# Kernel optimization log

Hardware: AMD Instinct MI355X
Metric: run time of the kernel (lower is better)

## Reference

```python
import jax, jax.numpy as jnp
import numpy as np

D_MODEL = 1024
N_HEAD = 16
D_K = D_MODEL // N_HEAD
B, S = 2, 2048
NEG = -1000000000.0


def setup_inputs() -> dict:
    key = jax.random.key(0)
    ks = jax.random.split(key, 9)
    inp = {
        "input_q": jax.random.normal(ks[0], (B, S, D_MODEL), dtype=jnp.float32),
        "input_k": jax.random.normal(ks[1], (B, S, D_MODEL), dtype=jnp.float32),
        "input_v": jax.random.normal(ks[2], (B, S, D_MODEL), dtype=jnp.float32),
        "mask": jax.random.randint(ks[3], (1, 1, S, S), 0, 2, dtype=jnp.int32),
        # parameters (Linear weights stored as [in, out] for x @ W)
        "w_q": jax.random.normal(ks[4], (D_MODEL, D_MODEL), dtype=jnp.float32) / np.sqrt(D_MODEL),
        "w_k": jax.random.normal(ks[5], (D_MODEL, D_MODEL), dtype=jnp.float32) / np.sqrt(D_MODEL),
        "w_v": jax.random.normal(ks[6], (D_MODEL, D_MODEL), dtype=jnp.float32) / np.sqrt(D_MODEL),
        "w_o": jax.random.normal(ks[7], (D_MODEL, D_MODEL), dtype=jnp.float32) / np.sqrt(D_MODEL),
        "b_o": jax.random.normal(ks[8], (D_MODEL,), dtype=jnp.float32) * 0.01,
    }
    return inp


def reference(input_q, input_k, input_v, mask, w_q, w_k, w_v, w_o, b_o):
    b = input_q.shape[0]
    # QKV projections -> [B, H, S, d_k]
    def split_heads(x):
        return x.reshape(b, -1, N_HEAD, D_K).transpose(0, 2, 1, 3)
    q = split_heads(input_q @ w_q)
    k = split_heads(input_k @ w_k)
    v = split_heads(input_v @ w_v)
    # naive attention: materialize [B, H, Sq, Sk] scores
    scores = jnp.einsum("bhqd,bhkd->bhqk", q, k) / jnp.sqrt(jnp.float32(D_K))
    scores = jnp.where(mask == 0, jnp.float32(NEG), scores)
    attn = jax.nn.softmax(scores, axis=-1)
    per_head = jnp.einsum("bhqk,bhkd->bhqd", attn, v)
    concat = per_head.transpose(0, 2, 1, 3).reshape(b, -1, N_HEAD * D_K)
    return concat @ w_o + b_o
```

## Files before the change

### kernel.cpp

```cpp
#include <hip/hip_runtime.h>
#include <hip/hip_bf16.h>

typedef _Float16 halfx8 __attribute__((ext_vector_type(8)));
typedef _Float16 halfx4 __attribute__((ext_vector_type(4)));
typedef _Float16 half2t __attribute__((ext_vector_type(2)));
typedef __fp16 fp16x2 __attribute__((ext_vector_type(2)));
typedef float floatx4 __attribute__((ext_vector_type(4)));

constexpr int S = 2048;
constexpr int DM = 1024;
constexpr int NH = 16;
constexpr int DK = 64;
constexpr int BATCH = 2;
constexpr int MROWS = 4096;
constexpr float QSCALE = 0.125f * 1.44269504088896340736f;

#if defined(__has_builtin)
#if __has_builtin(__builtin_amdgcn_fdot2)
#define HAVE_FDOT2 1
#endif
#if __has_builtin(__builtin_amdgcn_exp2f)
#define EXP2F(x) __builtin_amdgcn_exp2f(x)
#endif
#endif
#ifndef EXP2F
#define EXP2F(x) __builtin_exp2f(x)
#endif

static __device__ inline half2t pack2(float a, float b) {
  return __builtin_bit_cast(half2t, __builtin_amdgcn_cvt_pkrtz(a, b));
}

static __device__ inline float hdot2(half2t a, half2t b, float c) {
#ifdef HAVE_FDOT2
  return __builtin_amdgcn_fdot2(__builtin_bit_cast(fp16x2, a),
                                __builtin_bit_cast(fp16x2, b), c, false);
#else
  return c + (float)a[0] * (float)b[0] + (float)a[1] * (float)b[1];
#endif
}

static __device__ inline void load_lds16(const _Float16* g, _Float16* l) {
  __builtin_amdgcn_global_load_lds((const __attribute__((address_space(1))) void*)g,
                                   (__attribute__((address_space(3))) void*)l, 16, 0, 0);
}

__global__ void convert_w4(const float* __restrict__ w0, const float* __restrict__ w1,
                           const float* __restrict__ w2, const float* __restrict__ w3,
                           _Float16* __restrict__ o0, _Float16* __restrict__ o1,
                           _Float16* __restrict__ o2, _Float16* __restrict__ o3) {
  const float* w = (blockIdx.z == 0) ? w0 : (blockIdx.z == 1) ? w1 : (blockIdx.z == 2) ? w2 : w3;
  _Float16* wt = (blockIdx.z == 0) ? o0 : (blockIdx.z == 1) ? o1 : (blockIdx.z == 2) ? o2 : o3;
  __shared__ float tile[32][33];
  int n0 = blockIdx.x * 32, k0 = blockIdx.y * 32;
  int tx = threadIdx.x, ty = threadIdx.y;
#pragma unroll
  for (int i = 0; i < 4; ++i)
    tile[ty + i * 8][tx] = w[(k0 + ty + i * 8) * DM + n0 + tx];
  __syncthreads();
#pragma unroll
  for (int i = 0; i < 4; ++i)
    wt[(n0 + ty + i * 8) * DM + k0 + tx] = (_Float16)tile[tx][ty + i * 8];
}

__global__ void convert_in3(const float* __restrict__ a0, const float* __restrict__ a1,
                            const float* __restrict__ a2, _Float16* __restrict__ o0,
                            _Float16* __restrict__ o1, _Float16* __restrict__ o2) {
  const float* a = (blockIdx.z == 0) ? a0 : (blockIdx.z == 1) ? a1 : a2;
  _Float16* o = (blockIdx.z == 0) ? o0 : (blockIdx.z == 1) ? o1 : o2;
  size_t i = ((size_t)blockIdx.x * 256 + threadIdx.x) * 8;
  float4 va = *(const float4*)(a + i);
  float4 vb = *(const float4*)(a + i + 4);
  union { halfx8 v; _Float16 h[8]; } u;
  u.h[0] = (_Float16)va.x; u.h[1] = (_Float16)va.y;
  u.h[2] = (_Float16)va.z; u.h[3] = (_Float16)va.w;
  u.h[4] = (_Float16)vb.x; u.h[5] = (_Float16)vb.y;
  u.h[6] = (_Float16)vb.z; u.h[7] = (_Float16)vb.w;
  *(halfx8*)(o + i) = u.v;
}

__global__ void mask_swz(const int* __restrict__ m, _Float16* __restrict__ Mt) {
  int t = blockIdx.x * 256 + threadIdx.x;
  int j0 = (t & 1) * 8;
  int quad = (t >> 1) & 3;
  int q = (t >> 3) & (S - 1);
  int kt = t >> 14;
  const int* src = m + (size_t)q * S + kt * 64 + (j0 >> 2) * 16 + quad * 4;
  int4 a = *(const int4*)src;
  int4 b = *(const int4*)(src + 16);
  union { halfx8 v; _Float16 h[8]; } u;
  u.h[0] = (_Float16)(a.x != 0); u.h[1] = (_Float16)(a.y != 0);
  u.h[2] = (_Float16)(a.z != 0); u.h[3] = (_Float16)(a.w != 0);
  u.h[4] = (_Float16)(b.x != 0); u.h[5] = (_Float16)(b.y != 0);
  u.h[6] = (_Float16)(b.z != 0); u.h[7] = (_Float16)(b.w != 0);
  *(halfx8*)(Mt + (size_t)t * 8) = u.v;
}

__global__ __launch_bounds__(256) void qkv_gemm(const _Float16* __restrict__ xq,
                                                const _Float16* __restrict__ xk,
                                                const _Float16* __restrict__ xv,
                                                const _Float16* __restrict__ wqkv,
                                                _Float16* __restrict__ Qf,
                                                _Float16* __restrict__ Kf,
                                                _Float16* __restrict__ Vt) {
  __shared__ __align__(16) _Float16 smem[17408];
  _Float16* Asm = smem;
  _Float16* Bsm = smem + 128 * 64;
  const int tid = threadIdx.x;
  const int w = tid >> 6, l = tid & 63, lo = l & 15, quad = l >> 4;
  const int lo7 = l & 7;
  const int wm = (w >> 1) * 64, wn = (w & 1) * 64;
  const int bx = blockIdx.x, bm = blockIdx.y * 128;
  const int wid = bx >> 3;
  const _Float16* A = (wid == 0) ? xq : (wid == 1) ? xk : xv;
  const _Float16* Bt = wqkv + (size_t)bx * 128 * DM;

  floatx4 acc[4][4] = {};

  for (int k0 = 0; k0 < DM; k0 += 64) {
#pragma unroll
    for (int i = 0; i < 4; ++i) {
      int chunk = i * 256 + tid;
      int r = chunk >> 3;
      int c = (chunk & 7) ^ (r & 7);
      load_lds16(A + (size_t)(bm + r) * DM + k0 + c * 8, Asm + chunk * 8);
    }
#pragma unroll
    for (int i = 0; i < 4; ++i) {
      int chunk = i * 256 + tid;
      int r = chunk >> 3;
      int c = (chunk & 7) ^ (r & 7);
      load_lds16(Bt + (size_t)r * DM + k0 + c * 8, Bsm + chunk * 8);
    }
    __syncthreads();

#pragma unroll
    for (int ks = 0; ks < 2; ++ks) {
      halfx8 af[4], bf[4];
#pragma unroll
      for (int mt = 0; mt < 4; ++mt)
        af[mt] = *(const halfx8*)&Asm[(wm + mt * 16 + lo) * 64 + (((ks * 4 + quad) ^ lo7) * 8)];
#pragma unroll
      for (int nt = 0; nt < 4; ++nt)
        bf[nt] = *(const halfx8*)&Bsm[(wn + nt * 16 + lo) * 64 + (((ks * 4 + quad) ^ lo7) * 8)];
#pragma unroll
      for (int mt = 0; mt < 4; ++mt)
#pragma unroll
        for (int nt = 0; nt < 4; ++nt)
          acc[mt][nt] =
              __builtin_amdgcn_mfma_f32_16x16x32_f16(af[mt], bf[nt], acc[mt][nt], 0, 0, 0);
    }
    __syncthreads();
  }

  if (wid == 2) {
    constexpr int LDTT = 136;
    _Float16* tb = smem;
#pragma unroll
    for (int mt = 0; mt < 4; ++mt)
#pragma unroll
      for (int nt = 0; nt < 4; ++nt)
#pragma unroll
        for (int r = 0; r < 4; ++r) {
          int dl = wn + nt * 16 + lo;
          int sl = wm + mt * 16 + quad * 4 + r;
          tb[dl * LDTT + sl] = (_Float16)acc[mt][nt][r];
        }
    __syncthreads();
    const int b = bm >> 11, s0 = bm & (S - 1);
    const int d2 = tid >> 1, chunk = (tid & 1) * 64;
    const int dg = ((bx & 7) * 128 + d2);
    const int h = dg >> 6, dd = dg & 63;
    _Float16* O = Vt + ((size_t)(b * NH + h) * DK + dd) * S + s0 + chunk;
#pragma unroll
    for (int j = 0; j < 8; ++j)
      *(halfx8*)(O + j * 8) = *(const halfx8*)&tb[d2 * LDTT + chunk + j * 8];
    return;
  }

  _Float16* Out = (wid == 0) ? Qf : Kf;
  const float scale = (wid == 0) ? QSCALE : 1.0f;
#pragma unroll
  for (int mt = 0; mt < 4; ++mt)
#pragma unroll
    for (int nt = 0; nt < 4; ++nt)
#pragma unroll
      for (int r = 0; r < 4; ++r) {
        int row = bm + wm + mt * 16 + quad * 4 + r;
        int col = (bx & 7) * 128 + wn + nt * 16 + lo;
        Out[(size_t)row * DM + col] = (_Float16)(acc[mt][nt][r] * scale);
      }
}

__global__ __launch_bounds__(256, 2) void attn_kernel(const _Float16* __restrict__ Qf,
                                                      const _Float16* __restrict__ Kf,
                                                      const _Float16* __restrict__ Vt,
                                                      const _Float16* __restrict__ Mt,
                                                      _Float16* __restrict__ concat) {
  __shared__ __align__(16) _Float16 K0s[64 * 64], K1s[64 * 64];
  __shared__ __align__(16) _Float16 V0s[64 * 64], V1s[64 * 64];
  __shared__ __align__(16) _Float16 Psm[4 * 32 * 64];

  const int tid = threadIdx.x;
  const int w = tid >> 6, l = tid & 63, lo = l & 15, quad = l >> 4, lo7 = l & 7;
  const int qb = blockIdx.x * 128 + w * 32;
  const int h = blockIdx.y, b = blockIdx.z;

  const _Float16* Kbase = Kf + (size_t)b * S * DM + h * DK;
  const _Float16* Vb = Vt + (size_t)(b * NH + h) * DK * S;
  _Float16* Pw = Psm + w * 32 * 64;

  const int r0 = tid >> 3, c0 = (tid & 7) ^ (r0 & 7);
  const int r1 = (256 + tid) >> 3, c1 = ((256 + tid) & 7) ^ (r1 & 7);

  halfx8 qf[2][2];
  const _Float16* Mp[2];
#pragma unroll
  for (int g = 0; g < 2; ++g) {
#pragma unroll
    for (int ks = 0; ks < 2; ++ks)
      qf[g][ks] = *(const halfx8*)(Qf + ((size_t)b * S + qb + g * 16 + lo) * DM + h * DK +
                                   ks * 32 + quad * 8);
    Mp[g] = Mt + ((size_t)(qb + g * 16 + lo) * 4 + quad) * 16;
  }

  floatx4 Oacc[2][4] = {};
  float lsum[2] = {0.f, 0.f};
  const half2t onev = {(_Float16)1.0f, (_Float16)1.0f};

  auto stage = [&](int kt, _Float16* Kd, _Float16* Vd) {
    load_lds16(Kbase + (size_t)(kt * 64 + r0) * DM + c0 * 8, Kd + tid * 8);
    load_lds16(Vb + (size_t)r0 * S + kt * 64 + c0 * 8, Vd + tid * 8);
    load_lds16(Kbase + (size_t)(kt * 64 + r1) * DM + c1 * 8, Kd + (256 + tid) * 8);
    load_lds16(Vb + (size_t)r1 * S + kt * 64 + c1 * 8, Vd + (256 + tid) * 8);
  };

  auto tile = [&](const _Float16* Kc, const _Float16* Vc, const halfx8* mc) {
    floatx4 Sacc[2][4] = {};
#pragma unroll
    for (int ks = 0; ks < 2; ++ks)
#pragma unroll
      for (int nt = 0; nt < 4; ++nt) {
        halfx8 kf = *(const halfx8*)&Kc[(nt * 16 + lo) * 64 + (((ks * 4 + quad) ^ lo7) * 8)];
        Sacc[0][nt] = __builtin_amdgcn_mfma_f32_16x16x32_f16(kf, qf[0][ks], Sacc[0][nt], 0, 0, 0);
        Sacc[1][nt] = __builtin_amdgcn_mfma_f32_16x16x32_f16(kf, qf[1][ks], Sacc[1][nt], 0, 0, 0);
      }
#pragma unroll
    for (int g = 0; g < 2; ++g) {
      union { halfx8 v; half2t h2[4]; } mu0, mu1;
      mu0.v = mc[g * 2];
      mu1.v = mc[g * 2 + 1];
      half2t mm[8] = {mu0.h2[0], mu0.h2[1], mu0.h2[2], mu0.h2[3],
                      mu1.h2[0], mu1.h2[1], mu1.h2[2], mu1.h2[3]};
#pragma unroll
      for (int nt = 0; nt < 4; ++nt) {
        half2t p01 = pack2(EXP2F(Sacc[g][nt][0]), EXP2F(Sacc[g][nt][1]));
        half2t p23 = pack2(EXP2F(Sacc[g][nt][2]), EXP2F(Sacc[g][nt][3]));
        p01 *= mm[nt * 2];
        p23 *= mm[nt * 2 + 1];
        lsum[g] = hdot2(p01, onev, lsum[g]);
        lsum[g] = hdot2(p23, onev, lsum[g]);
        union { halfx4 v; half2t hh[2]; } u;
        u.hh[0] = p01;
        u.hh[1] = p23;
        *(halfx4*)&Pw[(g * 16 + lo) * 64 + (((2 * nt + (quad >> 1)) ^ lo7) * 8) +
                      (quad & 1) * 4] = u.v;
      }
    }
#pragma unroll
    for (int ks = 0; ks < 2; ++ks) {
      halfx8 pf0 = *(const halfx8*)&Pw[lo * 64 + (((ks * 4 + quad) ^ lo7) * 8)];
      halfx8 pf1 = *(const halfx8*)&Pw[(16 + lo) * 64 + (((ks * 4 + quad) ^ lo7) * 8)];
#pragma unroll
      for (int nt = 0; nt < 4; ++nt) {
        halfx8 vf = *(const halfx8*)&Vc[(nt * 16 + lo) * 64 + (((ks * 4 + quad) ^ lo7) * 8)];
        Oacc[0][nt] = __builtin_amdgcn_mfma_f32_16x16x32_f16(pf0, vf, Oacc[0][nt], 0, 0, 0);
        Oacc[1][nt] = __builtin_amdgcn_mfma_f32_16x16x32_f16(pf1, vf, Oacc[1][nt], 0, 0, 0);
      }
    }
  };

  halfx8 mr[4];
#pragma unroll
  for (int g = 0; g < 2; ++g) {
    mr[g * 2] = *(const halfx8*)(Mp[g]);
    mr[g * 2 + 1] = *(const halfx8*)(Mp[g] + 8);
  }
  stage(0, K0s, V0s);

  for (int kt = 0; kt < S / 64; kt += 2) {
    __syncthreads();
    stage(kt + 1, K1s, V1s);
    halfx8 mc[4] = {mr[0], mr[1], mr[2], mr[3]};
#pragma unroll
    for (int g = 0; g < 2; ++g) {
      mr[g * 2] = *(const halfx8*)(Mp[g] + (size_t)(kt + 1) * 131072);
      mr[g * 2 + 1] = *(const halfx8*)(Mp[g] + (size_t)(kt + 1) * 131072 + 8);
    }
    tile(K0s, V0s, mc);
    __syncthreads();
    if (kt + 2 < S / 64) stage(kt + 2, K0s, V0s);
    mc[0] = mr[0]; mc[1] = mr[1]; mc[2] = mr[2]; mc[3] = mr[3];
    if (kt + 2 < S / 64) {
#pragma unroll
      for (int g = 0; g < 2; ++g) {
        mr[g * 2] = *(const halfx8*)(Mp[g] + (size_t)(kt + 2) * 131072);
        mr[g * 2 + 1] = *(const halfx8*)(Mp[g] + (size_t)(kt + 2) * 131072 + 8);
      }
    }
    tile(K1s, V1s, mc);
  }

#pragma unroll
  for (int g = 0; g < 2; ++g) {
    lsum[g] += __shfl_xor(lsum[g], 16);
    lsum[g] += __shfl_xor(lsum[g], 32);
  }

#pragma unroll
  for (int g = 0; g < 2; ++g)
#pragma unroll
    for (int r = 0; r < 4; ++r) {
      float lr = __shfl(lsum[g], quad * 4 + r);
      float inv = __builtin_amdgcn_rcpf(lr);
      int q = qb + g * 16 + quad * 4 + r;
#pragma unroll
      for (int nt = 0; nt < 4; ++nt) {
        int d = nt * 16 + lo;
        concat[((size_t)b * S + q) * DM + h * DK + d] = (_Float16)(Oacc[g][nt][r] * inv);
      }
    }
}

__global__ __launch_bounds__(256) void out_gemm(const _Float16* __restrict__ A,
                                                const _Float16* __restrict__ Bt,
                                                float* __restrict__ Cp,
                                                const float* __restrict__ bias) {
  __shared__ __align__(16) _Float16 A0s[128 * 64], A1s[128 * 64];
  __shared__ __align__(16) _Float16 B0s[128 * 64], B1s[128 * 64];
  const int tid = threadIdx.x;
  const int w = tid >> 6, l = tid & 63, lo = l & 15, quad = l >> 4, lo7 = l & 7;
  const int wm = (w >> 1) * 64, wn = (w & 1) * 64;
  const int bm = blockIdx.y * 128, bn = blockIdx.x * 128;

  floatx4 acc[4][4] = {};

  auto stageg = [&](int k0, _Float16* Ad, _Float16* Bd) {
#pragma unroll
    for (int i = 0; i < 4; ++i) {
      int chunk = i * 256 + tid;
      int rr = chunk >> 3;
      int cc = (chunk & 7) ^ (rr & 7);
      load_lds16(A + (size_t)(bm + rr) * DM + k0 + cc * 8, Ad + chunk * 8);
      load_lds16(Bt + (size_t)(bn + rr) * DM + k0 + cc * 8, Bd + chunk * 8);
    }
  };
  auto comp = [&](const _Float16* As, const _Float16* Bs) {
#pragma unroll
    for (int ks = 0; ks < 2; ++ks) {
      halfx8 af[4], bf[4];
#pragma unroll
      for (int mt = 0; mt < 4; ++mt)
        af[mt] = *(const halfx8*)&As[(wm + mt * 16 + lo) * 64 + (((ks * 4 + quad) ^ lo7) * 8)];
#pragma unroll
      for (int nt = 0; nt < 4; ++nt)
        bf[nt] = *(const halfx8*)&Bs[(wn + nt * 16 + lo) * 64 + (((ks * 4 + quad) ^ lo7) * 8)];
#pragma unroll
      for (int mt = 0; mt < 4; ++mt)
#pragma unroll
        for (int nt = 0; nt < 4; ++nt)
          acc[mt][nt] =
              __builtin_amdgcn_mfma_f32_16x16x32_f16(af[mt], bf[nt], acc[mt][nt], 0, 0, 0);
    }
  };

  stageg(0, A0s, B0s);
  for (int k0 = 0; k0 < DM; k0 += 128) {
    __syncthreads();
    stageg(k0 + 64, A1s, B1s);
    comp(A0s, B0s);
    __syncthreads();
    if (k0 + 128 < DM) stageg(k0 + 128, A0s, B0s);
    comp(A1s, B1s);
  }

  float bv[4];
#pragma unroll
  for (int nt = 0; nt < 4; ++nt) bv[nt] = bias[bn + wn + nt * 16 + lo];
#pragma unroll
  for (int mt = 0; mt < 4; ++mt)
#pragma unroll
    for (int nt = 0; nt < 4; ++nt)
#pragma unroll
      for (int r = 0; r < 4; ++r) {
        int row = bm + wm + mt * 16 + quad * 4 + r;
        int col = bn + wn + nt * 16 + lo;
        Cp[(size_t)row * DM + col] = acc[mt][nt][r] + bv[nt];
      }
}

extern "C" void kernel_launch(void* const* d_in, const int* in_sizes, int n_in,
                              void* d_out, int out_size, void* d_ws, size_t ws_size,
                              hipStream_t stream) {
  const float* in_q = (const float*)d_in[0];
  const float* in_k = (const float*)d_in[1];
  const float* in_v = (const float*)d_in[2];
  const int* mask = (const int*)d_in[3];
  const float* w_q = (const float*)d_in[4];
  const float* w_k = (const float*)d_in[5];
  const float* w_v = (const float*)d_in[6];
  const float* w_o = (const float*)d_in[7];
  const float* b_o = (const float*)d_in[8];
  float* out = (float*)d_out;

  char* ws = (char*)d_ws;
  constexpr size_t WB = (size_t)DM * DM * sizeof(_Float16);
  constexpr size_t MB_ = (size_t)S * S * sizeof(_Float16);
  constexpr size_t TB = (size_t)MROWS * DM * sizeof(_Float16);
  _Float16* wqkv = (_Float16*)(ws);
  _Float16* wto = (_Float16*)(ws + 3 * WB);
  _Float16* Mt = (_Float16*)(ws + 4 * WB);
  char* p = ws + 4 * WB + MB_;
  _Float16* Qf = (_Float16*)(p);
  _Float16* Kf = (_Float16*)(p + TB);
  _Float16* Vt = (_Float16*)(p + 2 * TB);
  _Float16* xq = (_Float16*)(p + 3 * TB);
  _Float16* xk = (_Float16*)(p + 4 * TB);
  _Float16* xv = (_Float16*)(p + 5 * TB);
  _Float16* concat = xq;

  convert_w4<<<dim3(32, 32, 4), dim3(32, 8), 0, stream>>>(
      w_q, w_k, w_v, w_o, wqkv, wqkv + DM * DM, wqkv + 2 * DM * DM, wto);
  convert_in3<<<dim3(MROWS * DM / 8 / 256, 1, 3), 256, 0, stream>>>(in_q, in_k, in_v,
                                                                    xq, xk, xv);
  mask_swz<<<dim3(S * S / 8 / 256), 256, 0, stream>>>(mask, Mt);

  qkv_gemm<<<dim3(24, 32), 256, 0, stream>>>(xq, xk, xv, wqkv, Qf, Kf, Vt);
  attn_kernel<<<dim3(S / 128, NH, BATCH), 256, 0, stream>>>(Qf, Kf, Vt, Mt, concat);
  out_gemm<<<dim3(DM / 128, MROWS / 128), 256, 0, stream>>>(concat, wto, out, b_o);
}
```

Measured before the change: 250.7 us.

## Merge prep kernels and shrink attention and output-GEMM tiles for more blocks

Merges the three preprocessing kernels (weight transpose/convert, input convert, mask swizzle) into one launch that dispatches on block index, which removes two kernel launches. Cuts the attention block from 4 to 2 waves (64 query rows per block), doubling the grid to 1024 blocks, and narrows the output GEMM tile from 128 to 64 columns, doubling its grid to 512 blocks. The goal is better CU fill on a 256-CU part. The cost is less K/V and A-tile reuse per block and more global traffic.

```diff
diff --git a/kernel.cpp b/kernel.cpp
--- a/kernel.cpp
+++ b/kernel.cpp
@@ -45,55 +45,65 @@
                                    (__attribute__((address_space(3))) void*)l, 16, 0, 0);
 }
 
-__global__ void convert_w4(const float* __restrict__ w0, const float* __restrict__ w1,
-                           const float* __restrict__ w2, const float* __restrict__ w3,
-                           _Float16* __restrict__ o0, _Float16* __restrict__ o1,
-                           _Float16* __restrict__ o2, _Float16* __restrict__ o3) {
-  const float* w = (blockIdx.z == 0) ? w0 : (blockIdx.z == 1) ? w1 : (blockIdx.z == 2) ? w2 : w3;
-  _Float16* wt = (blockIdx.z == 0) ? o0 : (blockIdx.z == 1) ? o1 : (blockIdx.z == 2) ? o2 : o3;
+__global__ __launch_bounds__(256) void prep(const float* __restrict__ w_q,
+                                            const float* __restrict__ w_k,
+                                            const float* __restrict__ w_v,
+                                            const float* __restrict__ w_o,
+                                            _Float16* __restrict__ wqkv,
+                                            _Float16* __restrict__ wto,
+                                            const float* __restrict__ in_q,
+                                            const float* __restrict__ in_k,
+                                            const float* __restrict__ in_v,
+                                            _Float16* __restrict__ xq,
+                                            _Float16* __restrict__ xk,
+                                            _Float16* __restrict__ xv,
+                                            const int* __restrict__ mask,
+                                            _Float16* __restrict__ Mt) {
   __shared__ float tile[32][33];
-  int n0 = blockIdx.x * 32, k0 = blockIdx.y * 32;
-  int tx = threadIdx.x, ty = threadIdx.y;
-#pragma unroll
-  for (int i = 0; i < 4; ++i)
-    tile[ty + i * 8][tx] = w[(k0 + ty + i * 8) * DM + n0 + tx];
-  __syncthreads();
-#pragma unroll
-  for (int i = 0; i < 4; ++i)
-    wt[(n0 + ty + i * 8) * DM + k0 + tx] = (_Float16)tile[tx][ty + i * 8];
-}
-
-__global__ void convert_in3(const float* __restrict__ a0, const float* __restrict__ a1,
-                            const float* __restrict__ a2, _Float16* __restrict__ o0,
-                            _Float16* __restrict__ o1, _Float16* __restrict__ o2) {
-  const float* a = (blockIdx.z == 0) ? a0 : (blockIdx.z == 1) ? a1 : a2;
-  _Float16* o = (blockIdx.z == 0) ? o0 : (blockIdx.z == 1) ? o1 : o2;
-  size_t i = ((size_t)blockIdx.x * 256 + threadIdx.x) * 8;
-  float4 va = *(const float4*)(a + i);
-  float4 vb = *(const float4*)(a + i + 4);
-  union { halfx8 v; _Float16 h[8]; } u;
-  u.h[0] = (_Float16)va.x; u.h[1] = (_Float16)va.y;
-  u.h[2] = (_Float16)va.z; u.h[3] = (_Float16)va.w;
-  u.h[4] = (_Float16)vb.x; u.h[5] = (_Float16)vb.y;
-  u.h[6] = (_Float16)vb.z; u.h[7] = (_Float16)vb.w;
-  *(halfx8*)(o + i) = u.v;
-}
-
-__global__ void mask_swz(const int* __restrict__ m, _Float16* __restrict__ Mt) {
-  int t = blockIdx.x * 256 + threadIdx.x;
-  int j0 = (t & 1) * 8;
-  int quad = (t >> 1) & 3;
-  int q = (t >> 3) & (S - 1);
-  int kt = t >> 14;
-  const int* src = m + (size_t)q * S + kt * 64 + (j0 >> 2) * 16 + quad * 4;
-  int4 a = *(const int4*)src;
-  int4 b = *(const int4*)(src + 16);
-  union { halfx8 v; _Float16 h[8]; } u;
-  u.h[0] = (_Float16)(a.x != 0); u.h[1] = (_Float16)(a.y != 0);
-  u.h[2] = (_Float16)(a.z != 0); u.h[3] = (_Float16)(a.w != 0);
-  u.h[4] = (_Float16)(b.x != 0); u.h[5] = (_Float16)(b.y != 0);
-  u.h[6] = (_Float16)(b.z != 0); u.h[7] = (_Float16)(b.w != 0);
-  *(halfx8*)(Mt + (size_t)t * 8) = u.v;
+  const int bid = blockIdx.x;
+  const int tid = threadIdx.x;
+  if (bid < 4096) {
+    int wsel = bid >> 10, t = bid & 1023;
+    const float* w = (wsel == 0) ? w_q : (wsel == 1) ? w_k : (wsel == 2) ? w_v : w_o;
+    _Float16* wt = (wsel < 3) ? (wqkv + (size_t)wsel * DM * DM) : wto;
+    int n0 = (t & 31) * 32, k0 = (t >> 5) * 32;
+    int tx = tid & 31, ty = tid >> 5;
+#pragma unroll
+    for (int i = 0; i < 4; ++i)
+      tile[ty + i * 8][tx] = w[(size_t)(k0 + ty + i * 8) * DM + n0 + tx];
+    __syncthreads();
+#pragma unroll
+    for (int i = 0; i < 4; ++i)
+      wt[(size_t)(n0 + ty + i * 8) * DM + k0 + tx] = (_Float16)tile[tx][ty + i * 8];
+  } else if (bid < 10240) {
+    int idx = bid - 4096, isel = idx >> 11, blk = idx & 2047;
+    const float* a = (isel == 0) ? in_q : (isel == 1) ? in_k : in_v;
+    _Float16* o = (isel == 0) ? xq : (isel == 1) ? xk : xv;
+    size_t i = ((size_t)blk * 256 + tid) * 8;
+    float4 va = *(const float4*)(a + i);
+    float4 vb = *(const float4*)(a + i + 4);
+    union { halfx8 v; _Float16 h[8]; } u;
+    u.h[0] = (_Float16)va.x; u.h[1] = (_Float16)va.y;
+    u.h[2] = (_Float16)va.z; u.h[3] = (_Float16)va.w;
+    u.h[4] = (_Float16)vb.x; u.h[5] = (_Float16)vb.y;
+    u.h[6] = (_Float16)vb.z; u.h[7] = (_Float16)vb.w;
+    *(halfx8*)(o + i) = u.v;
+  } else {
+    int t = (bid - 10240) * 256 + tid;
+    int j0 = (t & 1) * 8;
+    int quad = (t >> 1) & 3;
+    int q = (t >> 3) & (S - 1);
+    int kt = t >> 14;
+    const int* src = mask + (size_t)q * S + kt * 64 + (j0 >> 2) * 16 + quad * 4;
+    int4 a = *(const int4*)src;
+    int4 b = *(const int4*)(src + 16);
+    union { halfx8 v; _Float16 h[8]; } u;
+    u.h[0] = (_Float16)(a.x != 0); u.h[1] = (_Float16)(a.y != 0);
+    u.h[2] = (_Float16)(a.z != 0); u.h[3] = (_Float16)(a.w != 0);
+    u.h[4] = (_Float16)(b.x != 0); u.h[5] = (_Float16)(b.y != 0);
+    u.h[6] = (_Float16)(b.z != 0); u.h[7] = (_Float16)(b.w != 0);
+    *(halfx8*)(Mt + (size_t)t * 8) = u.v;
+  }
 }
 
 __global__ __launch_bounds__(256) void qkv_gemm(const _Float16* __restrict__ xq,
@@ -192,26 +202,23 @@
       }
 }
 
-__global__ __launch_bounds__(256, 2) void attn_kernel(const _Float16* __restrict__ Qf,
+__global__ __launch_bounds__(128, 2) void attn_kernel(const _Float16* __restrict__ Qf,
                                                       const _Float16* __restrict__ Kf,
                                                       const _Float16* __restrict__ Vt,
                                                       const _Float16* __restrict__ Mt,
                                                       _Float16* __restrict__ concat) {
   __shared__ __align__(16) _Float16 K0s[64 * 64], K1s[64 * 64];
   __shared__ __align__(16) _Float16 V0s[64 * 64], V1s[64 * 64];
-  __shared__ __align__(16) _Float16 Psm[4 * 32 * 64];
+  __shared__ __align__(16) _Float16 Psm[2 * 32 * 64];
 
   const int tid = threadIdx.x;
   const int w = tid >> 6, l = tid & 63, lo = l & 15, quad = l >> 4, lo7 = l & 7;
-  const int qb = blockIdx.x * 128 + w * 32;
+  const int qb = blockIdx.x * 64 + w * 32;
   const int h = blockIdx.y, b = blockIdx.z;
 
   const _Float16* Kbase = Kf + (size_t)b * S * DM + h * DK;
   const _Float16* Vb = Vt + (size_t)(b * NH + h) * DK * S;
   _Float16* Pw = Psm + w * 32 * 64;
-
-  const int r0 = tid >> 3, c0 = (tid & 7) ^ (r0 & 7);
-  const int r1 = (256 + tid) >> 3, c1 = ((256 + tid) & 7) ^ (r1 & 7);
 
   halfx8 qf[2][2];
   const _Float16* Mp[2];
@@ -229,10 +236,14 @@
   const half2t onev = {(_Float16)1.0f, (_Float16)1.0f};
 
   auto stage = [&](int kt, _Float16* Kd, _Float16* Vd) {
-    load_lds16(Kbase + (size_t)(kt * 64 + r0) * DM + c0 * 8, Kd + tid * 8);
-    load_lds16(Vb + (size_t)r0 * S + kt * 64 + c0 * 8, Vd + tid * 8);
-    load_lds16(Kbase + (size_t)(kt * 64 + r1) * DM + c1 * 8, Kd + (256 + tid) * 8);
-    load_lds16(Vb + (size_t)r1 * S + kt * 64 + c1 * 8, Vd + (256 + tid) * 8);
+#pragma unroll
+    for (int i = 0; i < 4; ++i) {
+      int chunk = i * 128 + tid;
+      int r = chunk >> 3;
+      int c = (chunk & 7) ^ (r & 7);
+      load_lds16(Kbase + (size_t)(kt * 64 + r) * DM + c * 8, Kd + chunk * 8);
+      load_lds16(Vb + (size_t)r * S + kt * 64 + c * 8, Vd + chunk * 8);
+    }
   };
 
   auto tile = [&](const _Float16* Kc, const _Float16* Vc, const halfx8* mc) {
@@ -337,13 +348,13 @@
                                                 float* __restrict__ Cp,
                                                 const float* __restrict__ bias) {
   __shared__ __align__(16) _Float16 A0s[128 * 64], A1s[128 * 64];
-  __shared__ __align__(16) _Float16 B0s[128 * 64], B1s[128 * 64];
+  __shared__ __align__(16) _Float16 B0s[64 * 64], B1s[64 * 64];
   const int tid = threadIdx.x;
   const int w = tid >> 6, l = tid & 63, lo = l & 15, quad = l >> 4, lo7 = l & 7;
-  const int wm = (w >> 1) * 64, wn = (w & 1) * 64;
-  const int bm = blockIdx.y * 128, bn = blockIdx.x * 128;
-
-  floatx4 acc[4][4] = {};
+  const int wm = (w >> 1) * 64, wn = (w & 1) * 32;
+  const int bm = blockIdx.y * 128, bn = blockIdx.x * 64;
+
+  floatx4 acc[4][2] = {};
 
   auto stageg = [&](int k0, _Float16* Ad, _Float16* Bd) {
 #pragma unroll
@@ -352,23 +363,29 @@
       int rr = chunk >> 3;
       int cc = (chunk & 7) ^ (rr & 7);
       load_lds16(A + (size_t)(bm + rr) * DM + k0 + cc * 8, Ad + chunk * 8);
+    }
+#pragma unroll
+    for (int i = 0; i < 2; ++i) {
+      int chunk = i * 256 + tid;
+      int rr = chunk >> 3;
+      int cc = (chunk & 7) ^ (rr & 7);
       load_lds16(Bt + (size_t)(bn + rr) * DM + k0 + cc * 8, Bd + chunk * 8);
     }
   };
   auto comp = [&](const _Float16* As, const _Float16* Bs) {
 #pragma unroll
     for (int ks = 0; ks < 2; ++ks) {
-      halfx8 af[4], bf[4];
+      halfx8 af[4], bf[2];
 #pragma unroll
       for (int mt = 0; mt < 4; ++mt)
         af[mt] = *(const halfx8*)&As[(wm + mt * 16 + lo) * 64 + (((ks * 4 + quad) ^ lo7) * 8)];
 #pragma unroll
-      for (int nt = 0; nt < 4; ++nt)
+      for (int nt = 0; nt < 2; ++nt)
         bf[nt] = *(const halfx8*)&Bs[(wn + nt * 16 + lo) * 64 + (((ks * 4 + quad) ^ lo7) * 8)];
 #pragma unroll
       for (int mt = 0; mt < 4; ++mt)
 #pragma unroll
-        for (int nt = 0; nt < 4; ++nt)
+        for (int nt = 0; nt < 2; ++nt)
           acc[mt][nt] =
               __builtin_amdgcn_mfma_f32_16x16x32_f16(af[mt], bf[nt], acc[mt][nt], 0, 0, 0);
     }
@@ -384,13 +401,13 @@
     comp(A1s, B1s);
   }
 
-  float bv[4];
-#pragma unroll
-  for (int nt = 0; nt < 4; ++nt) bv[nt] = bias[bn + wn + nt * 16 + lo];
+  float bv[2];
+#pragma unroll
+  for (int nt = 0; nt < 2; ++nt) bv[nt] = bias[bn + wn + nt * 16 + lo];
 #pragma unroll
   for (int mt = 0; mt < 4; ++mt)
 #pragma unroll
-    for (int nt = 0; nt < 4; ++nt)
+    for (int nt = 0; nt < 2; ++nt)
 #pragma unroll
       for (int r = 0; r < 4; ++r) {
         int row = bm + wm + mt * 16 + quad * 4 + r;
@@ -429,13 +446,9 @@
   _Float16* xv = (_Float16*)(p + 5 * TB);
   _Float16* concat = xq;
 
-  convert_w4<<<dim3(32, 32, 4), dim3(32, 8), 0, stream>>>(
-      w_q, w_k, w_v, w_o, wqkv, wqkv + DM * DM, wqkv + 2 * DM * DM, wto);
-  convert_in3<<<dim3(MROWS * DM / 8 / 256, 1, 3), 256, 0, stream>>>(in_q, in_k, in_v,
-                                                                    xq, xk, xv);
-  mask_swz<<<dim3(S * S / 8 / 256), 256, 0, stream>>>(mask, Mt);
-
+  prep<<<dim3(12288), 256, 0, stream>>>(w_q, w_k, w_v, w_o, wqkv, wto,
+                                        in_q, in_k, in_v, xq, xk, xv, mask, Mt);
   qkv_gemm<<<dim3(24, 32), 256, 0, stream>>>(xq, xk, xv, wqkv, Qf, Kf, Vt);
-  attn_kernel<<<dim3(S / 128, NH, BATCH), 256, 0, stream>>>(Qf, Kf, Vt, Mt, concat);
-  out_gemm<<<dim3(DM / 128, MROWS / 128), 256, 0, stream>>>(concat, wto, out, b_o);
-}
+  attn_kernel<<<dim3(S / 64, NH, BATCH), 128, 0, stream>>>(Qf, Kf, Vt, Mt, concat);
+  out_gemm<<<dim3(DM / 64, MROWS / 128), 256, 0, stream>>>(concat, wto, out, b_o);
+}
```

Measured after the change: 245.7 us. 2.0% less time.
